# Kernel tuning notes

Hardware: AMD Instinct MI355X
Metric: run time of the kernel (lower is better)

## Reference

```python
import jax, jax.numpy as jnp
import numpy as np

B, C, H, W = 8, 512, 96, 96
CQ = C // 4


def setup_inputs() -> dict:
    key = jax.random.key(0)
    ks = jax.random.split(key, 8)
    s = 1.0 / np.sqrt(C)
    return {
        "x": jax.random.normal(ks[0], (B, C, H, W), jnp.float32),
        "Wq": jax.random.normal(ks[1], (CQ, C), jnp.float32) * s,
        "bq": jax.random.normal(ks[2], (CQ,), jnp.float32) * 0.01,
        "Wk": jax.random.normal(ks[3], (CQ, C), jnp.float32) * s,
        "bk": jax.random.normal(ks[4], (CQ,), jnp.float32) * 0.01,
        "Wv": jax.random.normal(ks[5], (C, C), jnp.float32) * s,
        "bv": jax.random.normal(ks[6], (C,), jnp.float32) * 0.01,
        "gamma": jax.random.normal(ks[7], (1,), jnp.float32) * 0.1,
    }


def _conv1x1(x, Wt, b):
    # 1x1 conv == per-pixel channel matmul: [B,C,H,W] x [O,C] -> [B,O,H,W]
    return jnp.einsum("bchw,oc->bohw", x, Wt) + b[None, :, None, None]


def reference(x, Wq, bq, Wk, bk, Wv, bv, gamma):
    b, c, h, w = x.shape
    q = _conv1x1(x, Wq, bq)  # [B,CQ,H,W]
    k = _conv1x1(x, Wk, bk)  # [B,CQ,H,W]
    v = _conv1x1(x, Wv, bv)  # [B,C ,H,W]

    # column (height-axis) attention energies, diagonal masked to -inf
    energy_H = jnp.einsum("bchw,bcjw->bhwj", q, k)  # [B,H,W,H]
    diag = jnp.eye(h, dtype=bool)[:, None, :]  # [H,1,H] broadcast over W
    energy_H = jnp.where(diag[None], -jnp.inf, energy_H)
    # row (width-axis) attention energies
    energy_W = jnp.einsum("bchw,bchj->bhwj", q, k)  # [B,H,W,W]

    att = jax.nn.softmax(jnp.concatenate([energy_H, energy_W], axis=3), axis=3)
    att_H = att[..., :h]       # [B,H,W,H]
    att_W = att[..., h:h + w]  # [B,H,W,W]

    out_H = jnp.einsum("bcjw,bhwj->bchw", v, att_H)
    out_W = jnp.einsum("bchj,bhwj->bchw", v, att_W)
    return gamma[0] * (out_H + out_W) + x
```

## Files before the change

kernel.cpp:

```cpp
#include <hip/hip_runtime.h>


#define B_ 8
#define C_ 512
#define CQ_ 128
#define H_ 96
#define W_ 96
#define HW_ 9216
#define J_ 192

typedef __attribute__((ext_vector_type(8))) short short8;
typedef __attribute__((ext_vector_type(4))) float f32x4;

__device__ __forceinline__ unsigned short f2bf(float f) {
    unsigned u = __float_as_uint(f);
    u += 0x7FFFu + ((u >> 16) & 1u);
    return (unsigned short)(u >> 16);
}
__device__ __forceinline__ float bf2f(unsigned short h) {
    return __uint_as_float((unsigned)h << 16);
}
__device__ __forceinline__ unsigned short f2h(float f) {
    _Float16 h = (_Float16)f;
    return __builtin_bit_cast(unsigned short, h);
}
__device__ __forceinline__ float h2f(unsigned short u) {
    return (float)__builtin_bit_cast(_Float16, u);
}
__device__ __forceinline__ void gl_lds16(const unsigned short* g, void* lds_base) {
    __builtin_amdgcn_global_load_lds((const __attribute__((address_space(1))) void*)g,
                                     (__attribute__((address_space(3))) void*)lds_base,
                                     16, 0, 0);
}

__global__ __launch_bounds__(256) void k0_wconv(const float* __restrict__ Wq,
                                                const float* __restrict__ Wk,
                                                const float* __restrict__ Wv,
                                                unsigned short* __restrict__ Wqk,
                                                unsigned short* __restrict__ Wvb) {
    int i = blockIdx.x * 256 + threadIdx.x;
    if (i < 65536)        Wqk[i] = f2bf(Wq[i]);
    else if (i < 131072)  Wqk[i] = f2bf(Wk[i - 65536]);
    else                  Wvb[i - 131072] = f2bf(Wv[i - 131072]);
}

__global__ __launch_bounds__(256) void k1_xT(const float* __restrict__ x,
                                             unsigned short* __restrict__ xT,
                                             unsigned short* __restrict__ xP) {
    __shared__ alignas(16) unsigned short tl[64][68];
    int b = blockIdx.z, c0 = blockIdx.y * 64, p0 = blockIdx.x * 64;
    int t = threadIdx.x;
    #pragma unroll
    for (int pass = 0; pass < 4; ++pass) {
        int m = t + pass * 256;
        int row = m >> 4, f4 = (m & 15) << 2;
        size_t off = ((size_t)(b * C_ + c0 + row)) * HW_ + p0 + f4;
        f32x4 v = *(const f32x4*)(x + off);
        uint2 o;
        o.x = (unsigned)f2bf(v[0]) | ((unsigned)f2bf(v[1]) << 16);
        o.y = (unsigned)f2bf(v[2]) | ((unsigned)f2bf(v[3]) << 16);
        *(uint2*)(xP + off) = o;
        *(uint2*)(&tl[row][f4]) = o;
    }
    __syncthreads();
    #pragma unroll
    for (int pass = 0; pass < 4; ++pass) {
        int m = t + pass * 256;
        int pr = m >> 4, cq = (m & 15) << 2;
        uint2 o;
        o.x = (unsigned)tl[cq + 0][pr] | ((unsigned)tl[cq + 1][pr] << 16);
        o.y = (unsigned)tl[cq + 2][pr] | ((unsigned)tl[cq + 3][pr] << 16);
        *(uint2*)(xT + ((size_t)(b * HW_ + p0 + pr)) * C_ + c0 + cq) = o;
    }
}

__global__ __launch_bounds__(256) void k3_vt(const unsigned short* __restrict__ src_,
                                             unsigned short* __restrict__ dst_) {
    __shared__ unsigned short tl[96][97];
    int plane = blockIdx.x;
    const unsigned short* src = src_ + (size_t)plane * HW_;
    unsigned short* dst = dst_ + (size_t)plane * HW_;
    int t = threadIdx.x;
    for (int m = t; m < 1152; m += 256) {
        int h = m / 12, w8 = (m % 12) * 8;
        uint4 v = *(const uint4*)(src + h * 96 + w8);
        tl[h][w8 + 0] = (unsigned short)(v.x);
        tl[h][w8 + 1] = (unsigned short)(v.x >> 16);
        tl[h][w8 + 2] = (unsigned short)(v.y);
        tl[h][w8 + 3] = (unsigned short)(v.y >> 16);
        tl[h][w8 + 4] = (unsigned short)(v.z);
        tl[h][w8 + 5] = (unsigned short)(v.z >> 16);
        tl[h][w8 + 6] = (unsigned short)(v.w);
        tl[h][w8 + 7] = (unsigned short)(v.w >> 16);
    }
    __syncthreads();
    for (int m = t; m < 1152; m += 256) {
        int w = m / 12, h8 = (m % 12) * 8;
        uint4 o;
        o.x = (unsigned)tl[h8 + 0][w] | ((unsigned)tl[h8 + 1][w] << 16);
        o.y = (unsigned)tl[h8 + 2][w] | ((unsigned)tl[h8 + 3][w] << 16);
        o.z = (unsigned)tl[h8 + 4][w] | ((unsigned)tl[h8 + 5][w] << 16);
        o.w = (unsigned)tl[h8 + 6][w] | ((unsigned)tl[h8 + 7][w] << 16);
        *(uint4*)(dst + w * 96 + h8) = o;
    }
}

__global__ __launch_bounds__(512) void k2a_qk(const unsigned short* __restrict__ xT,
                                              const unsigned short* __restrict__ Wqk,
                                              const float* __restrict__ bq,
                                              const float* __restrict__ bk,
                                              unsigned short* __restrict__ Qb,
                                              unsigned short* __restrict__ Kb) {
    __shared__ alignas(16) char smem[49152];
    unsigned short* AsBase = (unsigned short*)smem;
    unsigned short* BsBase = (unsigned short*)(smem + 16384);
    int t = threadIdx.x;
    int p0 = blockIdx.x * 128;
    int wid = t >> 6, lane = t & 63;
    int wr = wid >> 2, wc = wid & 3;
    int srow = lane >> 2;
    int sk8 = (((lane & 3) ^ (srow & 3)) << 3);
    const f32x4 zero = {0.f, 0.f, 0.f, 0.f};
    f32x4 acc[4][4];
    for (int m = 0; m < 4; ++m) for (int n = 0; n < 4; ++n) acc[m][n] = zero;

    auto STAGE = [&](int buf, int ks) {
        {
            int q = wid; int row = q * 16 + srow;
            gl_lds16(xT + ((size_t)(p0 + row) << 9) + ks + sk8,
                     smem + buf * 8192 + q * 1024);
        }
        #pragma unroll
        for (int i = 0; i < 2; ++i) {
            int q = wid * 2 + i; int row = q * 16 + srow;
            gl_lds16(Wqk + ((size_t)row << 9) + ks + sk8,
                     smem + 16384 + buf * 16384 + q * 1024);
        }
    };

    STAGE(0, 0);
    #pragma unroll
    for (int step = 0; step < 16; ++step) {
        int cur = step & 1;
        if (step < 15) {
            STAGE(cur ^ 1, (step + 1) * 32);
            asm volatile("s_waitcnt vmcnt(3)" ::: "memory");
        } else {
            asm volatile("s_waitcnt vmcnt(0)" ::: "memory");
        }
        __builtin_amdgcn_s_barrier();
        __builtin_amdgcn_sched_barrier(0);
        {
            short8 af[4], bfv[4];
            #pragma unroll
            for (int m = 0; m < 4; ++m) {
                int row = wr * 64 + m * 16 + (lane & 15);
                int po = (((lane >> 4) ^ (row & 3)) << 3);
                af[m] = *(const short8*)(AsBase + cur * 4096 + row * 32 + po);
            }
            #pragma unroll
            for (int n = 0; n < 4; ++n) {
                int row = wc * 64 + n * 16 + (lane & 15);
                int po = (((lane >> 4) ^ (row & 3)) << 3);
                bfv[n] = *(const short8*)(BsBase + cur * 8192 + row * 32 + po);
            }
            #pragma unroll
            for (int m = 0; m < 4; ++m)
                #pragma unroll
                for (int n = 0; n < 4; ++n)
                    acc[m][n] = __builtin_amdgcn_mfma_f32_16x16x32_bf16(af[m], bfv[n], acc[m][n], 0, 0, 0);
        }
        __builtin_amdgcn_s_barrier();
    }
    #pragma unroll
    for (int n = 0; n < 4; ++n) {
        int oc = wc * 64 + n * 16 + (lane & 15);
        float bias = (oc < 128) ? bq[oc] : bk[oc - 128];
        unsigned short* dst = (oc < 128) ? (Qb + oc) : (Kb + (oc - 128));
        #pragma unroll
        for (int m = 0; m < 4; ++m) {
            int pr = p0 + wr * 64 + m * 16 + ((lane >> 4) << 2);
            #pragma unroll
            for (int r = 0; r < 4; ++r)
                dst[(size_t)(pr + r) << 7] = f2bf(acc[m][n][r] + bias);
        }
    }
}

__global__ __launch_bounds__(256) void k4_energy(const unsigned short* __restrict__ Qb,
                                                 const unsigned short* __restrict__ Kb,
                                                 unsigned short* __restrict__ att) {
    __shared__ alignas(16) unsigned short Qs[96][136];
    __shared__ alignas(16) unsigned short Ks[96][136];
    int t = threadIdx.x;
    int modeH = blockIdx.z;
    int b = blockIdx.y, v0 = blockIdx.x;
    size_t base, rstride, obase_off, ostride;
    if (!modeH) {
        base      = (size_t)((b * H_ + v0) * W_) * CQ_;
        rstride   = CQ_;
        obase_off = (size_t)((b * H_ + v0) * W_) * J_ + H_;
        ostride   = J_;
    } else {
        base      = ((size_t)(b * H_) * W_ + v0) * CQ_;
        rstride   = (size_t)W_ * CQ_;
        obase_off = ((size_t)(b * H_) * W_ + v0) * J_;
        ostride   = (size_t)W_ * J_;
    }
    for (int q = t; q < 1536; q += 256) {
        int row = q >> 4, c8 = (q & 15) << 3;
        *(uint4*)(&Qs[row][c8]) = *(const uint4*)(Qb + base + (size_t)row * rstride + c8);
        *(uint4*)(&Ks[row][c8]) = *(const uint4*)(Kb + base + (size_t)row * rstride + c8);
    }
    __syncthreads();
    int wid = t >> 6, lane = t & 63;
    int wr = wid >> 1, wc = wid & 1;
    const f32x4 zero = {0.f, 0.f, 0.f, 0.f};
    f32x4 acc[3][3];
    for (int m = 0; m < 3; ++m) for (int n = 0; n < 3; ++n) acc[m][n] = zero;
    #pragma unroll
    for (int ks = 0; ks < 128; ks += 32) {
        int ko = ks + ((lane >> 4) << 3);
        short8 af[3], bfv[3];
        #pragma unroll
        for (int m = 0; m < 3; ++m) af[m] = *(const short8*)(&Qs[wr * 48 + m * 16 + (lane & 15)][ko]);
        #pragma unroll
        for (int n = 0; n < 3; ++n) bfv[n] = *(const short8*)(&Ks[wc * 48 + n * 16 + (lane & 15)][ko]);
        #pragma unroll
        for (int m = 0; m < 3; ++m)
            #pragma unroll
            for (int n = 0; n < 3; ++n)
                acc[m][n] = __builtin_amdgcn_mfma_f32_16x16x32_bf16(af[m], bfv[n], acc[m][n], 0, 0, 0);
    }
    unsigned short* ob = att + obase_off;
    #pragma unroll
    for (int m = 0; m < 3; ++m) {
        int i = wr * 48 + m * 16 + ((lane >> 4) << 2);
        #pragma unroll
        for (int n = 0; n < 3; ++n) {
            int j = wc * 48 + n * 16 + (lane & 15);
            #pragma unroll
            for (int r = 0; r < 4; ++r) {
                float v = acc[m][n][r];
                if (modeH && (i + r) == j) v = -__builtin_inff();
                ob[(size_t)(i + r) * ostride + j] = f2h(v);
            }
        }
    }
}

__global__ __launch_bounds__(256) void k5_softmax(const unsigned short* __restrict__ att,
                                                  unsigned short* __restrict__ att2) {
    int r = blockIdx.x * 4 + (threadIdx.x >> 6);
    int lane = threadIdx.x & 63;
    const unsigned short* row = att + (size_t)r * J_;
    float e0 = h2f(row[lane]), e1 = h2f(row[lane + 64]), e2 = h2f(row[lane + 128]);
    float m = fmaxf(e0, fmaxf(e1, e2));
    #pragma unroll
    for (int off = 32; off; off >>= 1) m = fmaxf(m, __shfl_xor(m, off, 64));
    float p0 = __expf(e0 - m), p1 = __expf(e1 - m), p2 = __expf(e2 - m);
    float s = p0 + p1 + p2;
    #pragma unroll
    for (int off = 32; off; off >>= 1) s += __shfl_xor(s, off, 64);
    float inv = 1.f / s;
    unsigned short* orow = att2 + (size_t)r * J_;
    orow[lane]       = f2bf(p0 * inv);
    orow[lane + 64]  = f2bf(p1 * inv);
    orow[lane + 128] = f2bf(p2 * inv);
}

template <int MODE>
__global__ __launch_bounds__(512) void k6_agg(const unsigned short* __restrict__ att2,
                                              const unsigned short* __restrict__ Xsrc,
                                              unsigned short* __restrict__ xAgg) {
    __shared__ alignas(16) unsigned short As[96][104];
    __shared__ alignas(16) unsigned short Bs[256][104];
    int t = threadIdx.x;
    int c0 = blockIdx.x * 256;
    int b = blockIdx.y / 96;
    int v = blockIdx.y % 96;
    size_t abase, astride;
    if (MODE == 0) { abase = ((size_t)(b * HW_) + (size_t)v * 96) * J_ + 96; astride = J_; }
    else           { abase = (size_t)(b * HW_) * J_ + (size_t)v * J_;        astride = (size_t)96 * J_; }
    if (t < 192) {
        int row = t >> 1, cs = (t & 1) * 6;
        const unsigned short* src = att2 + abase + (size_t)row * astride;
        #pragma unroll
        for (int i = 0; i < 6; ++i)
            *(uint4*)(&As[row][(cs + i) * 8]) = *(const uint4*)(src + (cs + i) * 8);
    }
    {
        int row = t >> 1, cs = (t & 1) * 6;
        const unsigned short* src = Xsrc + ((size_t)(b * C_) + c0 + row) * HW_ + v * 96;
        #pragma unroll
        for (int i = 0; i < 6; ++i)
            *(uint4*)(&Bs[row][(cs + i) * 8]) = *(const uint4*)(src + (cs + i) * 8);
    }
    __syncthreads();
    int wid = t >> 6, lane = t & 63;
    int wr = wid >> 2, wc = wid & 3;
    const f32x4 zero = {0.f, 0.f, 0.f, 0.f};
    f32x4 acc[3][4];
    for (int m = 0; m < 3; ++m) for (int n = 0; n < 4; ++n) acc[m][n] = zero;
    #pragma unroll
    for (int ks = 0; ks < 96; ks += 32) {
        int ko = ks + ((lane >> 4) << 3);
        short8 af[3], bfv[4];
        #pragma unroll
        for (int m = 0; m < 3; ++m) af[m] = *(const short8*)(&As[wr * 48 + m * 16 + (lane & 15)][ko]);
        #pragma unroll
        for (int n = 0; n < 4; ++n) bfv[n] = *(const short8*)(&Bs[wc * 64 + n * 16 + (lane & 15)][ko]);
        #pragma unroll
        for (int m = 0; m < 3; ++m)
            #pragma unroll
            for (int n = 0; n < 4; ++n)
                acc[m][n] = __builtin_amdgcn_mfma_f32_16x16x32_bf16(af[m], bfv[n], acc[m][n], 0, 0, 0);
    }
    #pragma unroll
    for (int m = 0; m < 3; ++m) {
        int orow = wr * 48 + m * 16 + ((lane >> 4) << 2);
        #pragma unroll
        for (int n = 0; n < 4; ++n) {
            int c = c0 + wc * 64 + n * 16 + (lane & 15);
            #pragma unroll
            for (int r = 0; r < 4; ++r) {
                int p = (MODE == 0) ? (v * 96 + orow + r) : ((orow + r) * 96 + v);
                size_t o = ((size_t)(b * HW_) + p) * C_ + c;
                if (MODE == 0) xAgg[o] = f2bf(acc[m][n][r]);
                else           xAgg[o] = f2bf(bf2f(xAgg[o]) + acc[m][n][r]);
            }
        }
    }
}

__global__ __launch_bounds__(256) void k9_proj(const unsigned short* __restrict__ xAgg,
                                               const unsigned short* __restrict__ Wvb,
                                               const float* __restrict__ bv,
                                               const unsigned short* __restrict__ xPb,
                                               const float* __restrict__ gamma_p,
                                               float* __restrict__ outp) {
    __shared__ alignas(16) char smem[32768];
    unsigned short* AsBase = (unsigned short*)smem;
    unsigned short* BsBase = (unsigned short*)(smem + 16384);
    int t = threadIdx.x;
    int bid = blockIdx.x;
    int tile = (bid & 7) * 288 + (bid >> 3);
    int oc0 = (tile & 3) * 128;
    int pt  = tile >> 2;
    int p0  = pt * 128;
    int wid = t >> 6, lane = t & 63;
    int wr = wid >> 1, wc = wid & 1;
    int srow = lane >> 2;
    int sk8 = (((lane & 3) ^ (srow & 3)) << 3);
    const f32x4 zero = {0.f, 0.f, 0.f, 0.f};
    f32x4 acc[4][4];
    for (int m = 0; m < 4; ++m) for (int n = 0; n < 4; ++n) acc[m][n] = zero;

    auto STAGE = [&](int buf, int ks) {
        #pragma unroll
        for (int i = 0; i < 2; ++i) {
            int q = wid * 2 + i; int row = q * 16 + srow;
            gl_lds16(Wvb + ((size_t)(oc0 + row) << 9) + ks + sk8,
                     smem + buf * 8192 + q * 1024);
        }
        #pragma unroll
        for (int i = 0; i < 2; ++i) {
            int q = wid * 2 + i; int row = q * 16 + srow;
            gl_lds16(xAgg + ((size_t)(p0 + row) << 9) + ks + sk8,
                     smem + 16384 + buf * 8192 + q * 1024);
        }
    };

    STAGE(0, 0);
    #pragma unroll
    for (int step = 0; step < 16; ++step) {
        int cur = step & 1;
        if (step < 15) {
            STAGE(cur ^ 1, (step + 1) * 32);
            asm volatile("s_waitcnt vmcnt(4)" ::: "memory");
        } else {
            asm volatile("s_waitcnt vmcnt(0)" ::: "memory");
        }
        __builtin_amdgcn_s_barrier();
        __builtin_amdgcn_sched_barrier(0);
        {
            short8 af[4], bfv[4];
            #pragma unroll
            for (int m = 0; m < 4; ++m) {
                int row = wr * 64 + m * 16 + (lane & 15);
                int po = (((lane >> 4) ^ (row & 3)) << 3);
                af[m] = *(const short8*)(AsBase + cur * 4096 + row * 32 + po);
            }
            #pragma unroll
            for (int n = 0; n < 4; ++n) {
                int row = wc * 64 + n * 16 + (lane & 15);
                int po = (((lane >> 4) ^ (row & 3)) << 3);
                bfv[n] = *(const short8*)(BsBase + cur * 4096 + row * 32 + po);
            }
            #pragma unroll
            for (int m = 0; m < 4; ++m)
                #pragma unroll
                for (int n = 0; n < 4; ++n)
                    acc[m][n] = __builtin_amdgcn_mfma_f32_16x16x32_bf16(af[m], bfv[n], acc[m][n], 0, 0, 0);
        }
        __builtin_amdgcn_s_barrier();
    }
    __syncthreads();

    #pragma unroll
    for (int m = 0; m < 4; ++m) {
        int rowb = wr * 64 + m * 16 + ((lane >> 4) << 2);
        #pragma unroll
        for (int r = 0; r < 4; ++r) {
            int row = rowb + r;
            float bias = bv[oc0 + row];
            #pragma unroll
            for (int n = 0; n < 4; ++n) {
                int col = wc * 64 + n * 16 + (lane & 15);
                int baddr = row * 256 + ((col << 1) ^ ((row & 7) << 4));
                *(unsigned short*)(smem + baddr) = f2bf(acc[m][n][r] + bias);
            }
        }
    }
    __syncthreads();

    int b = pt / 72;
    int hw0 = (pt % 72) * 128;
    float g = gamma_p[0];
    #pragma unroll
    for (int pass = 0; pass < 16; ++pass) {
        int row = pass * 8 + (t >> 5);
        int cs = (t & 31) * 4;
        uint2 tv = *(const uint2*)(smem + row * 256 + ((cs << 1) ^ ((row & 7) << 4)));
        int oc = oc0 + row;
        size_t o = ((size_t)(b * C_ + oc)) * HW_ + hw0 + cs;
        uint2 xv = *(const uint2*)(xPb + o);
        f32x4 ov;
        ov[0] = g * bf2f((unsigned short)(tv.x & 0xFFFF)) + bf2f((unsigned short)(xv.x & 0xFFFF));
        ov[1] = g * bf2f((unsigned short)(tv.x >> 16))    + bf2f((unsigned short)(xv.x >> 16));
        ov[2] = g * bf2f((unsigned short)(tv.y & 0xFFFF)) + bf2f((unsigned short)(xv.y & 0xFFFF));
        ov[3] = g * bf2f((unsigned short)(tv.y >> 16))    + bf2f((unsigned short)(xv.y >> 16));
        *(f32x4*)(outp + o) = ov;
    }
}

extern "C" void kernel_launch(void* const* d_in, const int* in_sizes, int n_in,
                              void* d_out, int out_size, void* d_ws, size_t ws_size,
                              hipStream_t stream) {
    const float* x  = (const float*)d_in[0];
    const float* Wq = (const float*)d_in[1];
    const float* bq = (const float*)d_in[2];
    const float* Wk = (const float*)d_in[3];
    const float* bk = (const float*)d_in[4];
    const float* Wv = (const float*)d_in[5];
    const float* bv = (const float*)d_in[6];
    const float* gm = (const float*)d_in[7];
    float* out = (float*)d_out;
    char* ws = (char*)d_ws;

    unsigned short* xT    = (unsigned short*)(ws + 0);
    unsigned short* xAgg  = (unsigned short*)(ws + 0);
    unsigned short* xP    = (unsigned short*)(ws + 75497472);
    unsigned short* Qb    = (unsigned short*)(ws + 150994944);
    unsigned short* att2  = (unsigned short*)(ws + 150994944);
    unsigned short* Kb    = (unsigned short*)(ws + 169869312);
    unsigned short* Wqk   = (unsigned short*)(ws + 188743680);
    unsigned short* Wvb   = (unsigned short*)(ws + 189005824);
    unsigned short* attf  = (unsigned short*)d_out;
    unsigned short* xPT   = (unsigned short*)((char*)d_out + 75497472);

    k0_wconv<<<1536, 256, 0, stream>>>(Wq, Wk, Wv, Wqk, Wvb);
    k1_xT<<<dim3(144, 8, 8), 256, 0, stream>>>(x, xT, xP);
    k2a_qk<<<576, 512, 0, stream>>>(xT, Wqk, bq, bk, Qb, Kb);
    k3_vt<<<4096, 256, 0, stream>>>(xP, xPT);
    k4_energy<<<dim3(96, 8, 2), 256, 0, stream>>>(Qb, Kb, attf);
    k5_softmax<<<18432, 256, 0, stream>>>(attf, att2);
    k6_agg<0><<<dim3(2, 768), 512, 0, stream>>>(att2, xP, xAgg);
    k6_agg<1><<<dim3(2, 768), 512, 0, stream>>>(att2, xPT, xAgg);
    k9_proj<<<2304, 256, 0, stream>>>(xAgg, Wvb, bv, xP, gm, out);
}
```

Measured before the change: 357.2 us.

## Store aggregated activations and Wv in FP8 and use FP8 MFMA projection

Converts Wv (scaled by 16) and the aggregated attention output xAgg to FP8 e4m3, halving the bytes written by the aggregation kernels and read by the projection GEMM. The projection now uses the fp8 16x16x32 MFMA with one 16-byte LDS load per operand row segment instead of two, and rescales by 1/16 at the end. The read-modify-write accumulation in the second aggregation pass now round-trips through FP8, which adds substantial quantization error to the attention output.

```diff
diff --git a/kernel.cpp b/kernel.cpp
--- a/kernel.cpp
+++ b/kernel.cpp
@@ -27,7 +27,13 @@
 __device__ __forceinline__ float h2f(unsigned short u) {
     return (float)__builtin_bit_cast(_Float16, u);
 }
-__device__ __forceinline__ void gl_lds16(const unsigned short* g, void* lds_base) {
+__device__ __forceinline__ unsigned char f2fp8(float v) {
+    return (unsigned char)(__builtin_amdgcn_cvt_pk_fp8_f32(v, 0.f, 0, 0) & 0xFF);
+}
+__device__ __forceinline__ float fp82f(unsigned char v) {
+    return __builtin_amdgcn_cvt_f32_fp8((int)v, 0);
+}
+__device__ __forceinline__ void gl_lds16(const void* g, void* lds_base) {
     __builtin_amdgcn_global_load_lds((const __attribute__((address_space(1))) void*)g,
                                      (__attribute__((address_space(3))) void*)lds_base,
                                      16, 0, 0);
@@ -37,11 +43,16 @@
                                                 const float* __restrict__ Wk,
                                                 const float* __restrict__ Wv,
                                                 unsigned short* __restrict__ Wqk,
-                                                unsigned short* __restrict__ Wvb) {
+                                                unsigned* __restrict__ Wv8u) {
     int i = blockIdx.x * 256 + threadIdx.x;
     if (i < 65536)        Wqk[i] = f2bf(Wq[i]);
     else if (i < 131072)  Wqk[i] = f2bf(Wk[i - 65536]);
-    else                  Wvb[i - 131072] = f2bf(Wv[i - 131072]);
+    else {
+        int j = (i - 131072) * 4;
+        int u = __builtin_amdgcn_cvt_pk_fp8_f32(Wv[j] * 16.f, Wv[j + 1] * 16.f, 0, 0);
+        u = __builtin_amdgcn_cvt_pk_fp8_f32(Wv[j + 2] * 16.f, Wv[j + 3] * 16.f, u, 1);
+        Wv8u[i - 131072] = (unsigned)u;
+    }
 }
 
 __global__ __launch_bounds__(256) void k1_xT(const float* __restrict__ x,
@@ -272,7 +283,7 @@
 template <int MODE>
 __global__ __launch_bounds__(512) void k6_agg(const unsigned short* __restrict__ att2,
                                               const unsigned short* __restrict__ Xsrc,
-                                              unsigned short* __restrict__ xAgg) {
+                                              unsigned char* __restrict__ xAgg8) {
     __shared__ alignas(16) unsigned short As[96][104];
     __shared__ alignas(16) unsigned short Bs[256][104];
     int t = threadIdx.x;
@@ -326,22 +337,20 @@
             for (int r = 0; r < 4; ++r) {
                 int p = (MODE == 0) ? (v * 96 + orow + r) : ((orow + r) * 96 + v);
                 size_t o = ((size_t)(b * HW_) + p) * C_ + c;
-                if (MODE == 0) xAgg[o] = f2bf(acc[m][n][r]);
-                else           xAgg[o] = f2bf(bf2f(xAgg[o]) + acc[m][n][r]);
-            }
-        }
-    }
-}
-
-__global__ __launch_bounds__(256) void k9_proj(const unsigned short* __restrict__ xAgg,
-                                               const unsigned short* __restrict__ Wvb,
+                if (MODE == 0) xAgg8[o] = f2fp8(acc[m][n][r]);
+                else           xAgg8[o] = f2fp8(fp82f(xAgg8[o]) + acc[m][n][r]);
+            }
+        }
+    }
+}
+
+__global__ __launch_bounds__(256) void k9_proj(const unsigned char* __restrict__ xAgg8,
+                                               const unsigned char* __restrict__ Wv8,
                                                const float* __restrict__ bv,
                                                const unsigned short* __restrict__ xPb,
                                                const float* __restrict__ gamma_p,
                                                float* __restrict__ outp) {
     __shared__ alignas(16) char smem[32768];
-    unsigned short* AsBase = (unsigned short*)smem;
-    unsigned short* BsBase = (unsigned short*)(smem + 16384);
     int t = threadIdx.x;
     int bid = blockIdx.x;
     int tile = (bid & 7) * 288 + (bid >> 3);
@@ -350,24 +359,22 @@
     int p0  = pt * 128;
     int wid = t >> 6, lane = t & 63;
     int wr = wid >> 1, wc = wid & 1;
-    int srow = lane >> 2;
-    int sk8 = (((lane & 3) ^ (srow & 3)) << 3);
+    int srow = lane >> 1;
+    int sb = (lane & 1) * 16;
     const f32x4 zero = {0.f, 0.f, 0.f, 0.f};
     f32x4 acc[4][4];
     for (int m = 0; m < 4; ++m) for (int n = 0; n < 4; ++n) acc[m][n] = zero;
 
     auto STAGE = [&](int buf, int ks) {
-        #pragma unroll
-        for (int i = 0; i < 2; ++i) {
-            int q = wid * 2 + i; int row = q * 16 + srow;
-            gl_lds16(Wvb + ((size_t)(oc0 + row) << 9) + ks + sk8,
-                     smem + buf * 8192 + q * 1024);
-        }
-        #pragma unroll
-        for (int i = 0; i < 2; ++i) {
-            int q = wid * 2 + i; int row = q * 16 + srow;
-            gl_lds16(xAgg + ((size_t)(p0 + row) << 9) + ks + sk8,
-                     smem + 16384 + buf * 8192 + q * 1024);
+        {
+            int q = wid; int row = q * 32 + srow;
+            gl_lds16(Wv8 + ((size_t)(oc0 + row) << 9) + ks + sb,
+                     smem + buf * 4096 + q * 1024);
+        }
+        {
+            int q = wid; int row = q * 32 + srow;
+            gl_lds16(xAgg8 + ((size_t)(p0 + row) << 9) + ks + sb,
+                     smem + 8192 + buf * 4096 + q * 1024);
         }
     };
 
@@ -377,31 +384,29 @@
         int cur = step & 1;
         if (step < 15) {
             STAGE(cur ^ 1, (step + 1) * 32);
-            asm volatile("s_waitcnt vmcnt(4)" ::: "memory");
+            asm volatile("s_waitcnt vmcnt(2)" ::: "memory");
         } else {
             asm volatile("s_waitcnt vmcnt(0)" ::: "memory");
         }
         __builtin_amdgcn_s_barrier();
         __builtin_amdgcn_sched_barrier(0);
         {
-            short8 af[4], bfv[4];
+            long af[4], bfv[4];
             #pragma unroll
             for (int m = 0; m < 4; ++m) {
                 int row = wr * 64 + m * 16 + (lane & 15);
-                int po = (((lane >> 4) ^ (row & 3)) << 3);
-                af[m] = *(const short8*)(AsBase + cur * 4096 + row * 32 + po);
+                af[m] = *(const long*)(smem + cur * 4096 + row * 32 + ((lane >> 4) << 3));
             }
             #pragma unroll
             for (int n = 0; n < 4; ++n) {
                 int row = wc * 64 + n * 16 + (lane & 15);
-                int po = (((lane >> 4) ^ (row & 3)) << 3);
-                bfv[n] = *(const short8*)(BsBase + cur * 4096 + row * 32 + po);
+                bfv[n] = *(const long*)(smem + 8192 + cur * 4096 + row * 32 + ((lane >> 4) << 3));
             }
             #pragma unroll
             for (int m = 0; m < 4; ++m)
                 #pragma unroll
                 for (int n = 0; n < 4; ++n)
-                    acc[m][n] = __builtin_amdgcn_mfma_f32_16x16x32_bf16(af[m], bfv[n], acc[m][n], 0, 0, 0);
+                    acc[m][n] = __builtin_amdgcn_mfma_f32_16x16x32_fp8_fp8(af[m], bfv[n], acc[m][n], 0, 0, 0);
         }
         __builtin_amdgcn_s_barrier();
     }
@@ -418,7 +423,7 @@
             for (int n = 0; n < 4; ++n) {
                 int col = wc * 64 + n * 16 + (lane & 15);
                 int baddr = row * 256 + ((col << 1) ^ ((row & 7) << 4));
-                *(unsigned short*)(smem + baddr) = f2bf(acc[m][n][r] + bias);
+                *(unsigned short*)(smem + baddr) = f2bf(acc[m][n][r] * 0.0625f + bias);
             }
         }
     }
@@ -459,23 +464,23 @@
     char* ws = (char*)d_ws;
 
     unsigned short* xT    = (unsigned short*)(ws + 0);
-    unsigned short* xAgg  = (unsigned short*)(ws + 0);
+    unsigned char*  xAgg8 = (unsigned char*)(ws + 0);
     unsigned short* xP    = (unsigned short*)(ws + 75497472);
     unsigned short* Qb    = (unsigned short*)(ws + 150994944);
     unsigned short* att2  = (unsigned short*)(ws + 150994944);
     unsigned short* Kb    = (unsigned short*)(ws + 169869312);
     unsigned short* Wqk   = (unsigned short*)(ws + 188743680);
-    unsigned short* Wvb   = (unsigned short*)(ws + 189005824);
+    unsigned*       Wv8u  = (unsigned*)(ws + 189005824);
     unsigned short* attf  = (unsigned short*)d_out;
     unsigned short* xPT   = (unsigned short*)((char*)d_out + 75497472);
 
-    k0_wconv<<<1536, 256, 0, stream>>>(Wq, Wk, Wv, Wqk, Wvb);
+    k0_wconv<<<768, 256, 0, stream>>>(Wq, Wk, Wv, Wqk, Wv8u);
     k1_xT<<<dim3(144, 8, 8), 256, 0, stream>>>(x, xT, xP);
     k2a_qk<<<576, 512, 0, stream>>>(xT, Wqk, bq, bk, Qb, Kb);
     k3_vt<<<4096, 256, 0, stream>>>(xP, xPT);
     k4_energy<<<dim3(96, 8, 2), 256, 0, stream>>>(Qb, Kb, attf);
     k5_softmax<<<18432, 256, 0, stream>>>(attf, att2);
-    k6_agg<0><<<dim3(2, 768), 512, 0, stream>>>(att2, xP, xAgg);
-    k6_agg<1><<<dim3(2, 768), 512, 0, stream>>>(att2, xPT, xAgg);
-    k9_proj<<<2304, 256, 0, stream>>>(xAgg, Wvb, bv, xP, gm, out);
-}
+    k6_agg<0><<<dim3(2, 768), 512, 0, stream>>>(att2, xP, xAgg8);
+    k6_agg<1><<<dim3(2, 768), 512, 0, stream>>>(att2, xPT, xAgg8);
+    k9_proj<<<2304, 256, 0, stream>>>(xAgg8, (const unsigned char*)Wv8u, bv, xP, gm, out);
+}
```

Result: faster. 341.5 us (-4.4%).
